# Optimization experiments

Measured on AMD Instinct MI355X. Metric: run time of the kernel, lower is better.

Reference implementation:

```python
import jax, jax.numpy as jnp
import numpy as np

B, C, H, W = 4, 64, 128, 128
NUM_HEAD = 1
SCALE = (C // NUM_HEAD) ** (-0.5)


def setup_inputs():
    key = jax.random.key(0)
    ks = jax.random.split(key, 32)
    def nrm(k, shape, s=0.05):
        return jax.random.normal(k, shape, jnp.float32) * s
    inp = {"x": jax.random.normal(ks[0], (B, C, H, W), jnp.float32)}
    i = 1
    for wn, bn in [("Wq", "bq"), ("Wk", "bk"), ("Wv", "bv"), ("Wl", "bl"), ("Wo", "bo"), ("Wp", "bp")]:
        inp[wn] = nrm(ks[i], (C, C)); i += 1
        inp[bn] = nrm(ks[i], (C,)); i += 1
    inp["sch_dw"] = nrm(ks[i], (C, 1, 5, 1)); i += 1
    inp["sch_dwb"] = nrm(ks[i], (C,)); i += 1
    inp["sch_pw"] = nrm(ks[i], (C, C, 1, 1)); i += 1
    inp["sch_pwb"] = nrm(ks[i], (C,)); i += 1
    inp["scv_dw"] = nrm(ks[i], (C, 1, 1, 5)); i += 1
    inp["scv_dwb"] = nrm(ks[i], (C,)); i += 1
    inp["scv_pw"] = nrm(ks[i], (C, C, 1, 1)); i += 1
    inp["scv_pwb"] = nrm(ks[i], (C,)); i += 1
    inp["convh_w"] = nrm(ks[i], (C, C, 1, 1)); i += 1
    inp["convh_b"] = nrm(ks[i], (C,)); i += 1
    inp["dsc_dw"] = nrm(ks[i], (C, 1, 3, 3)); i += 1
    inp["dsc_dwb"] = nrm(ks[i], (C,)); i += 1
    inp["dsc_pw"] = nrm(ks[i], (C, C, 1, 1)); i += 1
    inp["dsc_pwb"] = nrm(ks[i], (C,)); i += 1
    inp["ln_g"] = jnp.ones((C,), jnp.float32)
    inp["ln_b"] = jnp.zeros((C,), jnp.float32)
    return inp


def _linear(x, w, b):  # x [B,N,C], w [C,C] (torch Linear convention: y = x @ w.T + b)
    return x @ w.T + b


def _dwconv(x, w, b, pad):  # depthwise: x [B,C,H,W], w [C,1,kh,kw]
    y = jax.lax.conv_general_dilated(x, w, (1, 1), [(pad[0], pad[0]), (pad[1], pad[1])],
                                     dimension_numbers=("NCHW", "OIHW", "NCHW"),
                                     feature_group_count=x.shape[1])
    return y + b[None, :, None, None]


def _pwconv(x, w, b):  # 1x1 conv: w [Co,Ci,1,1]
    return jnp.einsum("bchw,oc->bohw", x, w[:, :, 0, 0]) + b[None, :, None, None]


def _attn(q, k, v):  # [B,N,C] each; dense NxN softmax attention
    a = jax.nn.softmax(jnp.einsum("bnc,bmc->bnm", q, k) * SCALE, axis=-1)
    return jnp.einsum("bnm,bmc->bnc", a, v)


def _up2_bilinear(x):  # bilinear, scale 2, align_corners=True
    Bb, Cc, Hh, Ww = x.shape
    def coords(n):
        s = jnp.linspace(0.0, n - 1.0, 2 * n)
        i0 = jnp.floor(s).astype(jnp.int32)
        i1 = jnp.minimum(i0 + 1, n - 1)
        return i0, i1, (s - i0).astype(x.dtype)
    y0, y1, wy = coords(Hh)
    x0, x1, wx = coords(Ww)
    r = x[:, :, y0, :] * (1.0 - wy)[None, None, :, None] + x[:, :, y1, :] * wy[None, None, :, None]
    return r[:, :, :, x0] * (1.0 - wx) + r[:, :, :, x1] * wx


def _forward(x, Wq, bq, Wk, bk, Wv, bv, Wl, bl, Wo, bo, Wp, bp,
             sch_dw, sch_dwb, sch_pw, sch_pwb, scv_dw, scv_dwb, scv_pw, scv_pwb,
             convh_w, convh_b, dsc_dw, dsc_dwb, dsc_pw, dsc_pwb, ln_g, ln_b):
    Bb, Cc, Hh, Ww = x.shape
    # AvgPool2d(2,2)
    xp = x.reshape(Bb, Cc, Hh // 2, 2, Ww // 2, 2).mean((3, 5))
    Hp, Wp_ = Hh // 2, Ww // 2
    N = Hp * Wp_
    # forward_lpg: GAP-gated self-attention producing low-freq prompt
    gap = xp.mean((2, 3), keepdims=True)
    xg = (gap * xp).reshape(Bb, Cc, N).transpose(0, 2, 1)  # [B,N,C]
    q = _linear(xg, Wq, bq); k = _linear(xg, Wk, bk); v = _linear(xg, Wv, bv)
    prompt_l = _linear(_attn(q, k, v), Wl, bl).transpose(0, 2, 1).reshape(Bb, Cc, Hp, Wp_)
    # forward_hpg: separable strip-conv branches -> high-freq prompt
    x_h = _pwconv(jax.nn.gelu(_dwconv(xp, sch_dw, sch_dwb, (2, 0)), approximate=False), sch_pw, sch_pwb)
    x_v = _pwconv(jax.nn.gelu(_dwconv(xp, scv_dw, scv_dwb, (0, 2)), approximate=False), scv_pw, scv_pwb)
    prompt_h = _pwconv(x_h + x_v, convh_w, convh_b)
    # forward_pgc: cross-attention Q=high, K=low, V=linear(x)
    x_V = _linear(xp.reshape(Bb, Cc, N).transpose(0, 2, 1), Wo, bo)
    x_K = prompt_l.reshape(Bb, Cc, N).transpose(0, 2, 1)
    x_Q = prompt_h.reshape(Bb, Cc, N).transpose(0, 2, 1)
    prompt = _attn(x_Q, x_K, x_V)
    prompt = _linear(prompt, Wp, bp) + x_V
    # LayerNorm over channel dim
    mu = prompt.mean(-1, keepdims=True)
    var = jnp.mean((prompt - mu) ** 2, axis=-1, keepdims=True)
    p_norm = (prompt - mu) / jnp.sqrt(var + 1e-5) * ln_g + ln_b
    p_norm = p_norm.transpose(0, 2, 1).reshape(Bb, Cc, Hp, Wp_)
    # dsc: depthwise 3x3 -> GELU -> 1x1, residual
    out = _pwconv(jax.nn.gelu(_dwconv(p_norm, dsc_dw, dsc_dwb, (1, 1)), approximate=False), dsc_pw, dsc_pwb) + p_norm
    return _up2_bilinear(out)


def reference(x, Wq, bq, Wk, bk, Wv, bv, Wl, bl, Wo, bo, Wp, bp,
              sch_dw, sch_dwb, sch_pw, sch_pwb, scv_dw, scv_dwb, scv_pw, scv_pwb,
              convh_w, convh_b, dsc_dw, dsc_dwb, dsc_pw, dsc_pwb, ln_g, ln_b):
    return _forward(x, Wq, bq, Wk, bk, Wv, bv, Wl, bl, Wo, bo, Wp, bp,
                    sch_dw, sch_dwb, sch_pw, sch_pwb, scv_dw, scv_dwb, scv_pw, scv_pwb,
                    convh_w, convh_b, dsc_dw, dsc_dwb, dsc_pw, dsc_pwb, ln_g, ln_b)
```

## Files before the change

### kernel.cpp

```cpp
#include <hip/hip_runtime.h>
#include <math.h>

#define Bn 4
#define Cn 64
#define Np 4096
#define NSPLIT 4
#define SCALE2 0.18033688011112042f

typedef unsigned short ushort_t;
typedef __attribute__((ext_vector_type(4))) float f32x4;
typedef __attribute__((ext_vector_type(8))) short bf16x8;
typedef __attribute__((ext_vector_type(4))) short bf16x4;

__device__ __forceinline__ float gelu_exact(float x) {
    return 0.5f * x * (1.0f + erff(x * 0.70710678118654752440f));
}
__device__ __forceinline__ ushort_t f2bf(float f) {
    unsigned int u = __float_as_uint(f);
    u += 0x7fffu + ((u >> 16) & 1u);
    return (ushort_t)(u >> 16);
}
__device__ __forceinline__ ushort_t f2bf_tr(float f) {
    return (ushort_t)(__float_as_uint(f) >> 16);
}
__device__ __forceinline__ float bf2f(ushort_t h) {
    return __uint_as_float(((unsigned int)h) << 16);
}
__device__ __forceinline__ void gload_lds16(const ushort_t* g, ushort_t* l) {
    __builtin_amdgcn_global_load_lds(
        (const __attribute__((address_space(1))) void*)g,
        (__attribute__((address_space(3))) void*)l, 16, 0, 0);
}
__device__ __forceinline__ bf16x8 cvt8(const float v[8]) {
    bf16x8 r;
    #pragma unroll
    for (int j = 0; j < 8; ++j) r[j] = (short)f2bf(v[j]);
    return r;
}
__device__ __forceinline__ void gemm16(const bf16x8 af[2], const float* __restrict__ W,
                                       int l16, int quad, f32x4* acc) {
    #pragma unroll
    for (int cb = 0; cb < 4; ++cb) {
        #pragma unroll
        for (int ks = 0; ks < 2; ++ks) {
            const float* p = W + (cb * 16 + l16) * 64 + ks * 32 + quad * 8;
            float v[8];
            #pragma unroll
            for (int j = 0; j < 8; ++j) v[j] = p[j];
            acc[cb] = __builtin_amdgcn_mfma_f32_16x16x32_bf16(af[ks], cvt8(v), acc[cb], 0, 0, 0);
        }
    }
}
__device__ __forceinline__ void gemm16T(const bf16x8 af[2], const float* __restrict__ W,
                                        int l16, int quad, f32x4* acc) {
    #pragma unroll
    for (int cb = 0; cb < 4; ++cb) {
        #pragma unroll
        for (int ks = 0; ks < 2; ++ks) {
            const float* p = W + (cb * 16 + l16) * 64 + ks * 32 + quad * 8;
            float v[8];
            #pragma unroll
            for (int j = 0; j < 8; ++j) v[j] = p[j];
            acc[cb] = __builtin_amdgcn_mfma_f32_16x16x32_bf16(cvt8(v), af[ks], acc[cb], 0, 0, 0);
        }
    }
}
__device__ __forceinline__ void aload(const float* xs, int row, int quad, bf16x8 af[2]) {
    #pragma unroll
    for (int ks = 0; ks < 2; ++ks) {
        float v[8];
        #pragma unroll
        for (int j = 0; j < 8; ++j) v[j] = xs[(ks * 32 + quad * 8 + j) * 65 + row];
        af[ks] = cvt8(v);
    }
}
__device__ __forceinline__ void stage_bchw(const float* __restrict__ X, int b, int n0, int t,
                                           float* xs) {
    #pragma unroll
    for (int u = 0; u < 16; ++u) {
        int idx = t + u * 256;
        int c = idx >> 6, nl = idx & 63;
        xs[c * 65 + nl] = X[((size_t)(b * Cn + c)) * Np + n0 + nl];
    }
}
__device__ __forceinline__ void stage_comb(const ushort_t* __restrict__ OpB, const float* linv,
                                           int b, int n0, int t, float* xs) {
    const size_t SS = (size_t)Bn * Np * Cn;
    int c4 = (t & 15) * 4;
    #pragma unroll
    for (int u = 0; u < 4; ++u) {
        int nl = (t >> 4) + u * 16;
        size_t gi = ((size_t)(b * Np + n0 + nl)) * Cn + c4;
        ushort4 a0 = *(const ushort4*)(OpB + gi);
        ushort4 a1 = *(const ushort4*)(OpB + SS + gi);
        ushort4 a2 = *(const ushort4*)(OpB + 2 * SS + gi);
        ushort4 a3 = *(const ushort4*)(OpB + 3 * SS + gi);
        float li = linv[nl];
        xs[(c4 + 0) * 65 + nl] = (bf2f(a0.x) + bf2f(a1.x) + bf2f(a2.x) + bf2f(a3.x)) * li;
        xs[(c4 + 1) * 65 + nl] = (bf2f(a0.y) + bf2f(a1.y) + bf2f(a2.y) + bf2f(a3.y)) * li;
        xs[(c4 + 2) * 65 + nl] = (bf2f(a0.z) + bf2f(a1.z) + bf2f(a2.z) + bf2f(a3.z)) * li;
        xs[(c4 + 3) * 65 + nl] = (bf2f(a0.w) + bf2f(a1.w) + bf2f(a2.w) + bf2f(a3.w)) * li;
    }
}
__device__ __forceinline__ void store_bnc_T(ushort_t* __restrict__ Y, int b, int n, int quad,
                                            const f32x4* acc, const float* __restrict__ bias,
                                            float mult) {
    #pragma unroll
    for (int cb = 0; cb < 4; ++cb) {
        int o0 = cb * 16 + quad * 4;
        ushort4 pk;
        pk.x = f2bf((acc[cb][0] + bias[o0 + 0]) * mult);
        pk.y = f2bf((acc[cb][1] + bias[o0 + 1]) * mult);
        pk.z = f2bf((acc[cb][2] + bias[o0 + 2]) * mult);
        pk.w = f2bf((acc[cb][3] + bias[o0 + 3]) * mult);
        *(ushort4*)(Y + ((size_t)(b * Np + n)) * Cn + o0) = pk;
    }
}
__device__ __forceinline__ void store_bchw_bf16(ushort_t* __restrict__ Y, int b, int nb, int l16,
                                                const f32x4* acc, const float* __restrict__ bias) {
    #pragma unroll
    for (int cb = 0; cb < 4; ++cb) {
        int col = cb * 16 + l16;
        float bb = bias[col];
        ushort4 pk;
        pk.x = f2bf(acc[cb][0] + bb); pk.y = f2bf(acc[cb][1] + bb);
        pk.z = f2bf(acc[cb][2] + bb); pk.w = f2bf(acc[cb][3] + bb);
        *(ushort4*)(Y + ((size_t)(b * Cn + col)) * Np + nb) = pk;
    }
}

__global__ void avgpool_kernel(const float* __restrict__ x, float* __restrict__ xp,
                               float* __restrict__ gap4k,
                               const float* __restrict__ convh_w, const float* __restrict__ convh_b,
                               const float* __restrict__ sch_pw, const float* __restrict__ sch_pwb,
                               const float* __restrict__ scv_pw, const float* __restrict__ scv_pwb,
                               float* __restrict__ Wc1, float* __restrict__ Wc2,
                               float* __restrict__ bcv) {
    if (blockIdx.x < 4096) {
        int idx = blockIdx.x * 256 + threadIdx.x;
        int j  = idx & 63;
        int i  = (idx >> 6) & 63;
        int bc = idx >> 12;
        const float* p = x + ((size_t)bc * 128 + 2 * i) * 128 + 2 * j;
        float v = 0.25f * (p[0] + p[1] + p[128] + p[129]);
        xp[idx] = v;
        float s = v;
        #pragma unroll
        for (int off = 1; off < 64; off <<= 1) s += __shfl_xor(s, off, 64);
        __shared__ float sm[4];
        if ((threadIdx.x & 63) == 0) sm[threadIdx.x >> 6] = s;
        __syncthreads();
        if (threadIdx.x == 0) gap4k[blockIdx.x] = sm[0] + sm[1] + sm[2] + sm[3];
    } else {
        int g = (blockIdx.x - 4096) * 256 + threadIdx.x;
        int sel = g >> 12, idx = g & 4095;
        int o = idx >> 6, c = idx & 63;
        const float* pw = sel ? scv_pw : sch_pw;
        float acc = 0.f;
        #pragma unroll 8
        for (int m = 0; m < 64; ++m) acc += convh_w[o * 64 + m] * pw[m * 64 + c];
        (sel ? Wc2 : Wc1)[idx] = acc * SCALE2;
        if (g < 64) {
            float ab = convh_b[g];
            for (int m = 0; m < 64; ++m) ab += convh_w[g * 64 + m] * (sch_pwb[m] + scv_pwb[m]);
            bcv[g] = ab * SCALE2;
        }
    }
}

__global__ __launch_bounds__(256) void qkv_dw_kernel(
    const float* __restrict__ xp, const float* __restrict__ gap4k,
    const float* __restrict__ Wq, const float* __restrict__ bq,
    const float* __restrict__ Wk, const float* __restrict__ bk,
    const float* __restrict__ Wv, const float* __restrict__ bv,
    const float* __restrict__ Wo, const float* __restrict__ bo,
    ushort_t* __restrict__ qb, ushort_t* __restrict__ kb, ushort_t* __restrict__ vb,
    float* __restrict__ xV, ushort_t* __restrict__ xVtb,
    const float* __restrict__ wv5, const float* __restrict__ bv5,
    const float* __restrict__ wh5, const float* __restrict__ bh5,
    ushort_t* __restrict__ gh, ushort_t* __restrict__ gv) {
    int b = blockIdx.y, t = threadIdx.x;
    if (blockIdx.x >= 64) {
        int part = blockIdx.x - 64;
        int e = part * 1024 + t * 4;
        size_t base = (size_t)b * (Cn * Np) + e;
        int c = e >> 12, i = (e >> 6) & 63, j = e & 63;
        const float* p = xp + ((size_t)(b * Cn + c)) * Np;
        float accV[4], accH[4];
        #pragma unroll
        for (int k = 0; k < 4; ++k) { accV[k] = bv5[c]; accH[k] = bh5[c]; }
        #pragma unroll
        for (int d = 0; d < 5; ++d) {
            int ii = i + d - 2;
            if (ii >= 0 && ii < 64) {
                f32x4 r = *(const f32x4*)(p + ii * 64 + j);
                float w = wv5[c * 5 + d];
                accV[0] += w * r[0]; accV[1] += w * r[1];
                accV[2] += w * r[2]; accV[3] += w * r[3];
            }
        }
        f32x4 c0 = *(const f32x4*)(p + i * 64 + j);
        float col[8];
        col[2] = c0[0]; col[3] = c0[1]; col[4] = c0[2]; col[5] = c0[3];
        col[0] = (j >= 2)     ? p[i * 64 + j - 2] : 0.f;
        col[1] = (j >= 1)     ? p[i * 64 + j - 1] : 0.f;
        col[6] = (j + 4 < 64) ? p[i * 64 + j + 4] : 0.f;
        col[7] = (j + 5 < 64) ? p[i * 64 + j + 5] : 0.f;
        #pragma unroll
        for (int k = 0; k < 4; ++k) {
            #pragma unroll
            for (int d = 0; d < 5; ++d) accH[k] += wh5[c * 5 + d] * col[k + d];
        }
        ushort4 ph, pv_;
        ph.x = f2bf(gelu_exact(accV[0])); ph.y = f2bf(gelu_exact(accV[1]));
        ph.z = f2bf(gelu_exact(accV[2])); ph.w = f2bf(gelu_exact(accV[3]));
        pv_.x = f2bf(gelu_exact(accH[0])); pv_.y = f2bf(gelu_exact(accH[1]));
        pv_.z = f2bf(gelu_exact(accH[2])); pv_.w = f2bf(gelu_exact(accH[3]));
        *(ushort4*)(gh + base) = ph;
        *(ushort4*)(gv + base) = pv_;
        return;
    }
    __shared__ float xs[64 * 65];
    __shared__ float gl[64];
    int n0 = blockIdx.x * 64;
    int wv_ = t >> 6, lane = t & 63, l16 = lane & 15, quad = lane >> 4;
    stage_bchw(xp, b, n0, t, xs);
    if (t < 64) {
        float s = 0.f;
        #pragma unroll
        for (int u = 0; u < 16; ++u) s += gap4k[(b * 64 + t) * 16 + u];
        gl[t] = s * (1.f / 4096.f);
    }
    __syncthreads();
    int row = wv_ * 16 + l16;
    int n   = n0 + wv_ * 16 + l16;
    int nb  = n0 + wv_ * 16 + quad * 4;
    bf16x8 ar[2], ag[2];
    #pragma unroll
    for (int ks = 0; ks < 2; ++ks) {
        float vr[8], vg[8];
        #pragma unroll
        for (int j = 0; j < 8; ++j) {
            int k = ks * 32 + quad * 8 + j;
            float xv = xs[k * 65 + row];
            vr[j] = xv; vg[j] = xv * gl[k];
        }
        ar[ks] = cvt8(vr); ag[ks] = cvt8(vg);
    }
    f32x4 acc[4];
    #pragma unroll
    for (int cb = 0; cb < 4; ++cb) acc[cb] = (f32x4){0.f, 0.f, 0.f, 0.f};
    gemm16T(ag, Wq, l16, quad, acc);
    store_bnc_T(qb, b, n, quad, acc, bq, SCALE2);
    #pragma unroll
    for (int cb = 0; cb < 4; ++cb) acc[cb] = (f32x4){0.f, 0.f, 0.f, 0.f};
    gemm16T(ag, Wk, l16, quad, acc);
    store_bnc_T(kb, b, n, quad, acc, bk, 1.f);
    #pragma unroll
    for (int cb = 0; cb < 4; ++cb) acc[cb] = (f32x4){0.f, 0.f, 0.f, 0.f};
    gemm16(ag, Wv, l16, quad, acc);
    store_bchw_bf16(vb, b, nb, l16, acc, bv);
    #pragma unroll
    for (int cb = 0; cb < 4; ++cb) acc[cb] = (f32x4){0.f, 0.f, 0.f, 0.f};
    gemm16(ar, Wo, l16, quad, acc);
    #pragma unroll
    for (int cb = 0; cb < 4; ++cb) {
        int col = cb * 16 + l16;
        float bb = bo[col];
        ushort4 pk;
        float y0 = acc[cb][0] + bb, y1 = acc[cb][1] + bb, y2 = acc[cb][2] + bb, y3 = acc[cb][3] + bb;
        xV[((size_t)(b * Np + nb + 0)) * Cn + col] = y0;
        xV[((size_t)(b * Np + nb + 1)) * Cn + col] = y1;
        xV[((size_t)(b * Np + nb + 2)) * Cn + col] = y2;
        xV[((size_t)(b * Np + nb + 3)) * Cn + col] = y3;
        pk.x = f2bf(y0); pk.y = f2bf(y1); pk.z = f2bf(y2); pk.w = f2bf(y3);
        *(ushort4*)(xVtb + ((size_t)(b * Cn + col)) * Np + nb) = pk;
    }
}

__device__ __forceinline__ void attn_body(
    int xblk, int b, const ushort_t* __restrict__ Qb, const ushort_t* __restrict__ Kb,
    const ushort_t* __restrict__ Vtb, ushort_t* __restrict__ OpB, float* __restrict__ Lpart,
    ushort_t* smem) {
    ushort_t* kt0 = smem;
    ushort_t* vt0 = smem + 8192;
    int split = xblk >> 6;
    int qt    = xblk & 63;
    int n0    = qt * 64;
    int t     = threadIdx.x;
    int wave  = t >> 6, lane = t & 63;
    int l16   = lane & 15, quad = lane >> 4;
    int lrow  = lane >> 3;
    int kvbase = split * (Np / NSPLIT);

    const ushort_t* qp = Qb + ((size_t)(b * Np) + n0 + wave * 16 + l16) * Cn + quad * 8;
    bf16x8 aq0 = *(const bf16x8*)(qp);
    bf16x8 aq1 = *(const bf16x8*)(qp + 32);

    f32x4 oa[4];
    float psum = 0.f;
    #pragma unroll
    for (int db = 0; db < 4; ++db) oa[db] = (f32x4){0.f, 0.f, 0.f, 0.f};

    int wh  = wave & 1;
    int jsw = ((lane & 7) ^ lrow) & 7;
    const ushort_t* gK  = Kb + ((size_t)b * Np + kvbase + wh * 32 + lrow) * Cn + jsw * 8;
    const ushort_t* gV0 = Vtb + ((size_t)(b * Cn) + wh * 32 + lrow) * Np + kvbase + jsw * 8;
    const ushort_t* gV1 = gV0 + (size_t)8 * Np;
    const ushort_t* gV2 = gV0 + (size_t)16 * Np;
    const ushort_t* gV3 = gV0 + (size_t)24 * Np;
    ushort_t* ldK = kt0 + wh * 2048;
    ushort_t* ldV = vt0 + wh * 2048;

    const ushort_t* kr0 = kt0 + l16 * 64 + ((quad ^ (l16 & 7)) & 7) * 8;
    const ushort_t* kr1 = kt0 + l16 * 64 + (((quad + 4) ^ (l16 & 7)) & 7) * 8;
    int h = quad >> 1, q1 = quad & 1, e = l16 & 7;
    const ushort_t* vr0 = vt0 + l16 * 64 + (((0 + h) ^ e) & 7) * 8 + q1 * 4;
    const ushort_t* vr1 = vt0 + l16 * 64 + (((2 + h) ^ e) & 7) * 8 + q1 * 4;
    const ushort_t* vr2 = vt0 + l16 * 64 + (((4 + h) ^ e) & 7) * 8 + q1 * 4;
    const ushort_t* vr3 = vt0 + l16 * 64 + (((6 + h) ^ e) & 7) * 8 + q1 * 4;

    auto stage = [&](int buf) {
        if (wave < 2) {
            ushort_t* dst = ldK + buf * 4096;
            gload_lds16(gK,        dst);
            gload_lds16(gK + 512,  dst + 512);
            gload_lds16(gK + 1024, dst + 1024);
            gload_lds16(gK + 1536, dst + 1536);
            gK += 64 * Cn;
        } else {
            ushort_t* dst = ldV + buf * 4096;
            gload_lds16(gV0, dst);
            gload_lds16(gV1, dst + 512);
            gload_lds16(gV2, dst + 1024);
            gload_lds16(gV3, dst + 1536);
            gV0 += 64; gV1 += 64; gV2 += 64; gV3 += 64;
        }
    };

    auto compute = [&](int B2) {
        const int ko = B2 * 4096;
        f32x4 sa[4];
        #pragma unroll
        for (int cb = 0; cb < 4; ++cb) sa[cb] = (f32x4){0.f, 0.f, 0.f, 0.f};
        #pragma unroll
        for (int cb = 0; cb < 4; ++cb) {
            bf16x8 bk0 = *(const bf16x8*)(kr0 + ko + cb * 1024);
            bf16x8 bk1 = *(const bf16x8*)(kr1 + ko + cb * 1024);
            sa[cb] = __builtin_amdgcn_mfma_f32_16x16x32_bf16(bk0, aq0, sa[cb], 0, 0, 0);
            sa[cb] = __builtin_amdgcn_mfma_f32_16x16x32_bf16(bk1, aq1, sa[cb], 0, 0, 0);
        }
        bf16x4 pb[4];
        #pragma unroll
        for (int cb = 0; cb < 4; ++cb) {
            float p0 = exp2f(sa[cb][0]), p1 = exp2f(sa[cb][1]);
            float p2 = exp2f(sa[cb][2]), p3 = exp2f(sa[cb][3]);
            psum += (p0 + p1) + (p2 + p3);
            bf16x4 pk;
            pk[0] = (short)f2bf_tr(p0); pk[1] = (short)f2bf_tr(p1);
            pk[2] = (short)f2bf_tr(p2); pk[3] = (short)f2bf_tr(p3);
            pb[cb] = pk;
        }
        #pragma unroll
        for (int db = 0; db < 4; ++db) {
            bf16x4 a0 = *(const bf16x4*)(vr0 + ko + db * 1024);
            bf16x4 a1 = *(const bf16x4*)(vr1 + ko + db * 1024);
            bf16x4 a2 = *(const bf16x4*)(vr2 + ko + db * 1024);
            bf16x4 a3 = *(const bf16x4*)(vr3 + ko + db * 1024);
            oa[db] = __builtin_amdgcn_mfma_f32_16x16x16bf16_1k(a0, pb[0], oa[db], 0, 0, 0);
            oa[db] = __builtin_amdgcn_mfma_f32_16x16x16bf16_1k(a1, pb[1], oa[db], 0, 0, 0);
            oa[db] = __builtin_amdgcn_mfma_f32_16x16x16bf16_1k(a2, pb[2], oa[db], 0, 0, 0);
            oa[db] = __builtin_amdgcn_mfma_f32_16x16x16bf16_1k(a3, pb[3], oa[db], 0, 0, 0);
        }
        __syncthreads();
    };

    const int NT = (Np / NSPLIT) / 64;
    stage(0);
    __syncthreads();
    #pragma unroll 1
    for (int mm = 0; mm < NT / 2; ++mm) {
        stage(1);
        compute(0);
        if (mm < NT / 2 - 1) stage(0);
        compute(1);
    }

    psum += __shfl_xor(psum, 16, 64);
    psum += __shfl_xor(psum, 32, 64);
    size_t obase = ((size_t)(split * Bn + b)) * Np;
    int n = n0 + wave * 16 + l16;
    if (quad == 0) Lpart[obase + n] = psum;
    #pragma unroll
    for (int db = 0; db < 4; ++db) {
        ushort4 pk;
        pk.x = f2bf(oa[db][0]); pk.y = f2bf(oa[db][1]);
        pk.z = f2bf(oa[db][2]); pk.w = f2bf(oa[db][3]);
        *(ushort4*)(OpB + (obase + n) * Cn + db * 16 + quad * 4) = pk;
    }
}

__device__ __forceinline__ void hpg_body(
    int tile, int b, const ushort_t* __restrict__ gh, const ushort_t* __restrict__ gv,
    const float* __restrict__ Wc1, const float* __restrict__ Wc2, const float* __restrict__ bcv,
    ushort_t* __restrict__ xQb, ushort_t* smem) {
    ushort_t* xs1 = smem;
    ushort_t* xs2 = smem + 4608;
    int n0 = tile * 64, t = threadIdx.x;
    int wv_ = t >> 6, lane = t & 63, l16 = lane & 15, quad = lane >> 4;
    #pragma unroll
    for (int u = 0; u < 4; ++u) {
        int lin = u * 256 + t;
        int c = lin >> 4, nl4 = (lin & 15) * 4;
        size_t gi = ((size_t)(b * Cn + c)) * Np + n0 + nl4;
        ushort4 g1 = *(const ushort4*)(gh + gi);
        ushort4 g2 = *(const ushort4*)(gv + gi);
        xs1[(nl4 + 0) * 72 + c] = g1.x; xs1[(nl4 + 1) * 72 + c] = g1.y;
        xs1[(nl4 + 2) * 72 + c] = g1.z; xs1[(nl4 + 3) * 72 + c] = g1.w;
        xs2[(nl4 + 0) * 72 + c] = g2.x; xs2[(nl4 + 1) * 72 + c] = g2.y;
        xs2[(nl4 + 2) * 72 + c] = g2.z; xs2[(nl4 + 3) * 72 + c] = g2.w;
    }
    __syncthreads();
    int row = wv_ * 16 + l16;
    bf16x8 a1[2], a2[2];
    #pragma unroll
    for (int ks = 0; ks < 2; ++ks) {
        a1[ks] = *(const bf16x8*)(xs1 + row * 72 + ks * 32 + quad * 8);
        a2[ks] = *(const bf16x8*)(xs2 + row * 72 + ks * 32 + quad * 8);
    }
    f32x4 acc[4];
    #pragma unroll
    for (int cb = 0; cb < 4; ++cb) acc[cb] = (f32x4){0.f, 0.f, 0.f, 0.f};
    gemm16T(a1, Wc1, l16, quad, acc);
    gemm16T(a2, Wc2, l16, quad, acc);
    store_bnc_T(xQb, b, n0 + wv_ * 16 + l16, quad, acc, bcv, 1.f);
}

__global__ __launch_bounds__(256) void attn_hpg_kernel(
    const ushort_t* __restrict__ Qb, const ushort_t* __restrict__ Kb,
    const ushort_t* __restrict__ Vtb, ushort_t* __restrict__ OpB, float* __restrict__ Lpart,
    const ushort_t* __restrict__ gh, const ushort_t* __restrict__ gv,
    const float* __restrict__ Wc1, const float* __restrict__ Wc2,
    const float* __restrict__ bcv, ushort_t* __restrict__ xQb) {
    __shared__ ushort_t smem[16384];
    int b = blockIdx.y;
    if (blockIdx.x < 256)
        attn_body(blockIdx.x, b, Qb, Kb, Vtb, OpB, Lpart, smem);
    else
        hpg_body(blockIdx.x - 256, b, gh, gv, Wc1, Wc2, bcv, xQb, smem);
}

__global__ __launch_bounds__(256) void wl_mfma(
    const ushort_t* __restrict__ OpB, const float* __restrict__ Lp,
    const float* __restrict__ Wl, const float* __restrict__ bl, ushort_t* __restrict__ xKb) {
    __shared__ float xs[64 * 65];
    __shared__ float linv[64];
    int b = blockIdx.y, n0 = blockIdx.x * 64, t = threadIdx.x;
    int wv_ = t >> 6, lane = t & 63, l16 = lane & 15, quad = lane >> 4;
    if (t < 64) {
        size_t li = (size_t)b * Np + n0 + t;
        const size_t LS = (size_t)Bn * Np;
        linv[t] = 1.f / (Lp[li] + Lp[LS + li] + Lp[2 * LS + li] + Lp[3 * LS + li]);
    }
    __syncthreads();
    stage_comb(OpB, linv, b, n0, t, xs);
    __syncthreads();
    bf16x8 af[2];
    aload(xs, wv_ * 16 + l16, quad, af);
    f32x4 acc[4];
    #pragma unroll
    for (int cb = 0; cb < 4; ++cb) acc[cb] = (f32x4){0.f, 0.f, 0.f, 0.f};
    gemm16T(af, Wl, l16, quad, acc);
    store_bnc_T(xKb, b, n0 + wv_ * 16 + l16, quad, acc, bl, 1.f);
}

__global__ __launch_bounds__(256) void linln_mfma(
    const ushort_t* __restrict__ OpB, const float* __restrict__ Lp,
    const float* __restrict__ Wp, const float* __restrict__ bp,
    const float* __restrict__ xV, const float* __restrict__ g, const float* __restrict__ beta,
    float* __restrict__ out) {
    __shared__ float xs[64 * 65];
    __shared__ float linv[64];
    int b = blockIdx.y, n0 = blockIdx.x * 64, t = threadIdx.x;
    int wv_ = t >> 6, lane = t & 63, l16 = lane & 15, quad = lane >> 4;
    if (t < 64) {
        size_t li = (size_t)b * Np + n0 + t;
        const size_t LS = (size_t)Bn * Np;
        linv[t] = 1.f / (Lp[li] + Lp[LS + li] + Lp[2 * LS + li] + Lp[3 * LS + li]);
    }
    __syncthreads();
    stage_comb(OpB, linv, b, n0, t, xs);
    __syncthreads();
    bf16x8 af[2];
    aload(xs, wv_ * 16 + l16, quad, af);
    f32x4 acc[4];
    #pragma unroll
    for (int cb = 0; cb < 4; ++cb) acc[cb] = (f32x4){0.f, 0.f, 0.f, 0.f};
    gemm16(af, Wp, l16, quad, acc);
    int nb = n0 + wv_ * 16 + quad * 4;
    float vals[4][4], gc[4], bec[4];
    #pragma unroll
    for (int cb = 0; cb < 4; ++cb) {
        int col = cb * 16 + l16;
        float bb = bp[col];
        gc[cb] = g[col]; bec[cb] = beta[col];
        #pragma unroll
        for (int r = 0; r < 4; ++r)
            vals[cb][r] = acc[cb][r] + bb + xV[((size_t)(b * Np + nb + r)) * Cn + col];
    }
    f32x4 yn[4];
    #pragma unroll
    for (int r = 0; r < 4; ++r) {
        float s = 0.f, s2 = 0.f;
        #pragma unroll
        for (int cb = 0; cb < 4; ++cb) { s += vals[cb][r]; s2 += vals[cb][r] * vals[cb][r]; }
        #pragma unroll
        for (int off = 1; off < 16; off <<= 1) {
            s  += __shfl_xor(s, off, 64);
            s2 += __shfl_xor(s2, off, 64);
        }
        float mu  = s * (1.f / 64.f);
        float var = s2 * (1.f / 64.f) - mu * mu;
        float ivs = rsqrtf(var + 1e-5f);
        #pragma unroll
        for (int cb = 0; cb < 4; ++cb)
            yn[cb][r] = (vals[cb][r] - mu) * ivs * gc[cb] + bec[cb];
    }
    #pragma unroll
    for (int cb = 0; cb < 4; ++cb)
        *(f32x4*)(out + ((size_t)(b * Cn + cb * 16 + l16)) * Np + nb) = yn[cb];
}

__global__ __launch_bounds__(256) void dsc_mfma(
    const float* __restrict__ X, const float* __restrict__ dw, const float* __restrict__ dwb,
    const float* __restrict__ W, const float* __restrict__ bias, float* __restrict__ out) {
    __shared__ float xs[64 * 65];
    int b = blockIdx.y, irow = blockIdx.x, n0 = irow * 64, t = threadIdx.x;
    int wv_ = t >> 6, lane = t & 63, l16 = lane & 15, quad = lane >> 4;
    int j = t & 63;
    #pragma unroll
    for (int u = 0; u < 16; ++u) {
        int c = (t >> 6) + u * 4;
        const float* p = X + ((size_t)(b * Cn + c)) * Np + n0;
        float acc = dwb[c];
        #pragma unroll
        for (int dy = 0; dy < 3; ++dy) {
            int ii = irow + dy - 1;
            if (ii < 0 || ii >= 64) continue;
            const float* pr = p + (dy - 1) * 64;
            #pragma unroll
            for (int dx = 0; dx < 3; ++dx) {
                int jj = j + dx - 1;
                if (jj < 0 || jj >= 64) continue;
                acc += dw[c * 9 + dy * 3 + dx] * pr[jj];
            }
        }
        xs[c * 65 + j] = gelu_exact(acc);
    }
    __syncthreads();
    bf16x8 af[2];
    aload(xs, wv_ * 16 + l16, quad, af);
    f32x4 acc[4];
    #pragma unroll
    for (int cb = 0; cb < 4; ++cb) acc[cb] = (f32x4){0.f, 0.f, 0.f, 0.f};
    gemm16(af, W, l16, quad, acc);
    int nb = n0 + wv_ * 16 + quad * 4;
    #pragma unroll
    for (int cb = 0; cb < 4; ++cb) {
        int col = cb * 16 + l16;
        float bb = bias[col];
        size_t oi = ((size_t)(b * Cn + col)) * Np + nb;
        f32x4 rv = *(const f32x4*)(X + oi);
        f32x4 v4;
        #pragma unroll
        for (int r = 0; r < 4; ++r) v4[r] = acc[cb][r] + bb + rv[r];
        *(f32x4*)(out + oi) = v4;
    }
}

__global__ void upsample_kernel(const float* __restrict__ in, float* __restrict__ out) {
    int idx = blockIdx.x * 256 + threadIdx.x;
    int x4 = (idx & 31) * 4;
    int y  = (idx >> 5) & 127;
    int bc = idx >> 12;
    float sy = y * (63.f / 127.f);
    int y0 = (int)sy;
    float fy = sy - y0;
    int y1 = min(y0 + 1, 63);
    const float* p0 = in + (size_t)bc * Np + y0 * 64;
    const float* p1 = in + (size_t)bc * Np + y1 * 64;
    f32x4 o;
    #pragma unroll
    for (int k = 0; k < 4; ++k) {
        int xo = x4 + k;
        float sx = xo * (63.f / 127.f);
        int x0 = (int)sx;
        float fx = sx - x0;
        int x1 = min(x0 + 1, 63);
        float r0 = p0[x0] + (p0[x1] - p0[x0]) * fx;
        float r1 = p1[x0] + (p1[x1] - p1[x0]) * fx;
        o[k] = r0 + (r1 - r0) * fy;
    }
    *(f32x4*)(out + (size_t)idx * 4) = o;
}

extern "C" void kernel_launch(void* const* d_in, const int* in_sizes, int n_in,
                              void* d_out, int out_size, void* d_ws, size_t ws_size,
                              hipStream_t stream) {
    const float* x       = (const float*)d_in[0];
    const float* Wq      = (const float*)d_in[1];
    const float* bq      = (const float*)d_in[2];
    const float* Wk      = (const float*)d_in[3];
    const float* bk      = (const float*)d_in[4];
    const float* Wv      = (const float*)d_in[5];
    const float* bv      = (const float*)d_in[6];
    const float* Wl      = (const float*)d_in[7];
    const float* bl      = (const float*)d_in[8];
    const float* Wo      = (const float*)d_in[9];
    const float* bo      = (const float*)d_in[10];
    const float* Wp      = (const float*)d_in[11];
    const float* bp      = (const float*)d_in[12];
    const float* sch_dw  = (const float*)d_in[13];
    const float* sch_dwb = (const float*)d_in[14];
    const float* sch_pw  = (const float*)d_in[15];
    const float* sch_pwb = (const float*)d_in[16];
    const float* scv_dw  = (const float*)d_in[17];
    const float* scv_dwb = (const float*)d_in[18];
    const float* scv_pw  = (const float*)d_in[19];
    const float* scv_pwb = (const float*)d_in[20];
    const float* convh_w = (const float*)d_in[21];
    const float* convh_b = (const float*)d_in[22];
    const float* dsc_dw  = (const float*)d_in[23];
    const float* dsc_dwb = (const float*)d_in[24];
    const float* dsc_pw  = (const float*)d_in[25];
    const float* dsc_pwb = (const float*)d_in[26];
    const float* ln_g    = (const float*)d_in[27];
    const float* ln_b    = (const float*)d_in[28];

    float* ws = (float*)d_ws;
    const size_t SZ = (size_t)Bn * Np * Cn;
    float* xp   = ws;
    float* xV   = ws + SZ;
    ushort_t* ghb = (ushort_t*)(ws + 2 * SZ);
    ushort_t* gh  = ghb;
    ushort_t* gv  = ghb + SZ;
    float* f2   = ws + 2 * SZ;
    ushort_t* bws  = (ushort_t*)(ws + 3 * SZ);
    ushort_t* qb   = bws;
    ushort_t* kb_  = bws + SZ;
    ushort_t* vb   = bws + 2 * SZ;
    ushort_t* xKb  = bws + 3 * SZ;
    ushort_t* xVtb = bws + 4 * SZ;
    ushort_t* xQb  = bws + 5 * SZ;
    ushort_t* OpB  = (ushort_t*)(ws + 6 * SZ);
    float* gap4k  = ws + 8 * SZ;
    float* Lpart  = gap4k + 4096;
    float* Wc1  = Lpart + (size_t)NSPLIT * Bn * Np;
    float* Wc2  = Wc1 + 4096;
    float* bcv  = Wc2 + 4096;

    dim3 g64(64, Bn);

    avgpool_kernel<<<4096 + 32, 256, 0, stream>>>(x, xp, gap4k,
                                                  convh_w, convh_b, sch_pw, sch_pwb,
                                                  scv_pw, scv_pwb, Wc1, Wc2, bcv);
    qkv_dw_kernel<<<dim3(64 + 256, Bn), 256, 0, stream>>>(
        xp, gap4k, Wq, bq, Wk, bk, Wv, bv, Wo, bo,
        qb, kb_, vb, xV, xVtb, sch_dw, sch_dwb, scv_dw, scv_dwb, gh, gv);
    attn_hpg_kernel<<<dim3(256 + 64, Bn), 256, 0, stream>>>(
        qb, kb_, vb, OpB, Lpart, gh, gv, Wc1, Wc2, bcv, xQb);
    wl_mfma<<<g64, 256, 0, stream>>>(OpB, Lpart, Wl, bl, xKb);
    attn_hpg_kernel<<<dim3(256, Bn), 256, 0, stream>>>(
        xQb, xKb, xVtb, OpB, Lpart, gh, gv, Wc1, Wc2, bcv, xQb);
    linln_mfma<<<g64, 256, 0, stream>>>(OpB, Lpart, Wp, bp, xV, ln_g, ln_b, xp);
    dsc_mfma<<<g64, 256, 0, stream>>>(xp, dsc_dw, dsc_dwb, dsc_pw, dsc_pwb, f2);
    upsample_kernel<<<4096, 256, 0, stream>>>(f2, (float*)d_out);
}
```

Before: 265.1 us.

## Double attention query tile per block and pre-convert weights to bf16

The attention body now processes 128 query rows per block, so each wave handles two 16-row query tiles that share every K/V fragment loaded from shared memory. This halves the number of attention blocks and the K/V staging traffic per query. Separately, all 64x64 projection weights are converted to bf16 once in the first kernel, so GEMMs load packed bf16 vectors instead of eight floats followed by a conversion. The cost is higher register pressure from the doubled accumulators, which may lower occupancy, and fewer blocks to fill the device.

```diff
diff --git a/kernel.cpp b/kernel.cpp
--- a/kernel.cpp
+++ b/kernel.cpp
@@ -37,31 +37,25 @@
     for (int j = 0; j < 8; ++j) r[j] = (short)f2bf(v[j]);
     return r;
 }
-__device__ __forceinline__ void gemm16(const bf16x8 af[2], const float* __restrict__ W,
-                                       int l16, int quad, f32x4* acc) {
+__device__ __forceinline__ void gemm16b(const bf16x8 af[2], const ushort_t* __restrict__ Wb,
+                                        int l16, int quad, f32x4* acc) {
     #pragma unroll
     for (int cb = 0; cb < 4; ++cb) {
         #pragma unroll
         for (int ks = 0; ks < 2; ++ks) {
-            const float* p = W + (cb * 16 + l16) * 64 + ks * 32 + quad * 8;
-            float v[8];
-            #pragma unroll
-            for (int j = 0; j < 8; ++j) v[j] = p[j];
-            acc[cb] = __builtin_amdgcn_mfma_f32_16x16x32_bf16(af[ks], cvt8(v), acc[cb], 0, 0, 0);
-        }
-    }
-}
-__device__ __forceinline__ void gemm16T(const bf16x8 af[2], const float* __restrict__ W,
-                                        int l16, int quad, f32x4* acc) {
+            bf16x8 bw = *(const bf16x8*)(Wb + (cb * 16 + l16) * 64 + ks * 32 + quad * 8);
+            acc[cb] = __builtin_amdgcn_mfma_f32_16x16x32_bf16(af[ks], bw, acc[cb], 0, 0, 0);
+        }
+    }
+}
+__device__ __forceinline__ void gemm16Tb(const bf16x8 af[2], const ushort_t* __restrict__ Wb,
+                                         int l16, int quad, f32x4* acc) {
     #pragma unroll
     for (int cb = 0; cb < 4; ++cb) {
         #pragma unroll
         for (int ks = 0; ks < 2; ++ks) {
-            const float* p = W + (cb * 16 + l16) * 64 + ks * 32 + quad * 8;
-            float v[8];
-            #pragma unroll
-            for (int j = 0; j < 8; ++j) v[j] = p[j];
-            acc[cb] = __builtin_amdgcn_mfma_f32_16x16x32_bf16(cvt8(v), af[ks], acc[cb], 0, 0, 0);
+            bf16x8 bw = *(const bf16x8*)(Wb + (cb * 16 + l16) * 64 + ks * 32 + quad * 8);
+            acc[cb] = __builtin_amdgcn_mfma_f32_16x16x32_bf16(bw, af[ks], acc[cb], 0, 0, 0);
         }
     }
 }
@@ -134,8 +128,12 @@
                                const float* __restrict__ convh_w, const float* __restrict__ convh_b,
                                const float* __restrict__ sch_pw, const float* __restrict__ sch_pwb,
                                const float* __restrict__ scv_pw, const float* __restrict__ scv_pwb,
-                               float* __restrict__ Wc1, float* __restrict__ Wc2,
-                               float* __restrict__ bcv) {
+                               ushort_t* __restrict__ Wc1b, ushort_t* __restrict__ Wc2b,
+                               float* __restrict__ bcv,
+                               const float* __restrict__ Wq, const float* __restrict__ Wk,
+                               const float* __restrict__ Wv, const float* __restrict__ Wo,
+                               const float* __restrict__ Wl, const float* __restrict__ Wp,
+                               const float* __restrict__ dscpw, ushort_t* __restrict__ Wball) {
     if (blockIdx.x < 4096) {
         int idx = blockIdx.x * 256 + threadIdx.x;
         int j  = idx & 63;
@@ -151,7 +149,7 @@
         if ((threadIdx.x & 63) == 0) sm[threadIdx.x >> 6] = s;
         __syncthreads();
         if (threadIdx.x == 0) gap4k[blockIdx.x] = sm[0] + sm[1] + sm[2] + sm[3];
-    } else {
+    } else if (blockIdx.x < 4128) {
         int g = (blockIdx.x - 4096) * 256 + threadIdx.x;
         int sel = g >> 12, idx = g & 4095;
         int o = idx >> 6, c = idx & 63;
@@ -159,21 +157,26 @@
         float acc = 0.f;
         #pragma unroll 8
         for (int m = 0; m < 64; ++m) acc += convh_w[o * 64 + m] * pw[m * 64 + c];
-        (sel ? Wc2 : Wc1)[idx] = acc * SCALE2;
+        (sel ? Wc2b : Wc1b)[idx] = f2bf(acc * SCALE2);
         if (g < 64) {
             float ab = convh_b[g];
             for (int m = 0; m < 64; ++m) ab += convh_w[g * 64 + m] * (sch_pwb[m] + scv_pwb[m]);
             bcv[g] = ab * SCALE2;
         }
+    } else {
+        int g = (blockIdx.x - 4128) * 256 + threadIdx.x;
+        int which = g >> 12, idx = g & 4095;
+        const float* srcs[7] = {Wq, Wk, Wv, Wo, Wl, Wp, dscpw};
+        Wball[g] = f2bf(srcs[which][idx]);
     }
 }
 
 __global__ __launch_bounds__(256) void qkv_dw_kernel(
     const float* __restrict__ xp, const float* __restrict__ gap4k,
-    const float* __restrict__ Wq, const float* __restrict__ bq,
-    const float* __restrict__ Wk, const float* __restrict__ bk,
-    const float* __restrict__ Wv, const float* __restrict__ bv,
-    const float* __restrict__ Wo, const float* __restrict__ bo,
+    const ushort_t* __restrict__ Wqb, const float* __restrict__ bq,
+    const ushort_t* __restrict__ Wkb, const float* __restrict__ bk,
+    const ushort_t* __restrict__ Wvb, const float* __restrict__ bv,
+    const ushort_t* __restrict__ Wob, const float* __restrict__ bo,
     ushort_t* __restrict__ qb, ushort_t* __restrict__ kb, ushort_t* __restrict__ vb,
     float* __restrict__ xV, ushort_t* __restrict__ xVtb,
     const float* __restrict__ wv5, const float* __restrict__ bv5,
@@ -250,19 +253,19 @@
     f32x4 acc[4];
     #pragma unroll
     for (int cb = 0; cb < 4; ++cb) acc[cb] = (f32x4){0.f, 0.f, 0.f, 0.f};
-    gemm16T(ag, Wq, l16, quad, acc);
+    gemm16Tb(ag, Wqb, l16, quad, acc);
     store_bnc_T(qb, b, n, quad, acc, bq, SCALE2);
     #pragma unroll
     for (int cb = 0; cb < 4; ++cb) acc[cb] = (f32x4){0.f, 0.f, 0.f, 0.f};
-    gemm16T(ag, Wk, l16, quad, acc);
+    gemm16Tb(ag, Wkb, l16, quad, acc);
     store_bnc_T(kb, b, n, quad, acc, bk, 1.f);
     #pragma unroll
     for (int cb = 0; cb < 4; ++cb) acc[cb] = (f32x4){0.f, 0.f, 0.f, 0.f};
-    gemm16(ag, Wv, l16, quad, acc);
+    gemm16b(ag, Wvb, l16, quad, acc);
     store_bchw_bf16(vb, b, nb, l16, acc, bv);
     #pragma unroll
     for (int cb = 0; cb < 4; ++cb) acc[cb] = (f32x4){0.f, 0.f, 0.f, 0.f};
-    gemm16(ar, Wo, l16, quad, acc);
+    gemm16b(ar, Wob, l16, quad, acc);
     #pragma unroll
     for (int cb = 0; cb < 4; ++cb) {
         int col = cb * 16 + l16;
@@ -284,23 +287,28 @@
     ushort_t* smem) {
     ushort_t* kt0 = smem;
     ushort_t* vt0 = smem + 8192;
-    int split = xblk >> 6;
-    int qt    = xblk & 63;
-    int n0    = qt * 64;
+    int split = xblk >> 5;
+    int qt    = xblk & 31;
+    int n0    = qt * 128;
     int t     = threadIdx.x;
     int wave  = t >> 6, lane = t & 63;
     int l16   = lane & 15, quad = lane >> 4;
     int lrow  = lane >> 3;
     int kvbase = split * (Np / NSPLIT);
 
-    const ushort_t* qp = Qb + ((size_t)(b * Np) + n0 + wave * 16 + l16) * Cn + quad * 8;
-    bf16x8 aq0 = *(const bf16x8*)(qp);
-    bf16x8 aq1 = *(const bf16x8*)(qp + 32);
-
-    f32x4 oa[4];
-    float psum = 0.f;
-    #pragma unroll
-    for (int db = 0; db < 4; ++db) oa[db] = (f32x4){0.f, 0.f, 0.f, 0.f};
+    const ushort_t* qp = Qb + ((size_t)(b * Np) + n0 + wave * 32 + l16) * Cn + quad * 8;
+    bf16x8 aq00 = *(const bf16x8*)(qp);
+    bf16x8 aq01 = *(const bf16x8*)(qp + 32);
+    bf16x8 aq10 = *(const bf16x8*)(qp + 16 * Cn);
+    bf16x8 aq11 = *(const bf16x8*)(qp + 16 * Cn + 32);
+
+    f32x4 oa0[4], oa1[4];
+    float psum0 = 0.f, psum1 = 0.f;
+    #pragma unroll
+    for (int db = 0; db < 4; ++db) {
+        oa0[db] = (f32x4){0.f, 0.f, 0.f, 0.f};
+        oa1[db] = (f32x4){0.f, 0.f, 0.f, 0.f};
+    }
 
     int wh  = wave & 1;
     int jsw = ((lane & 7) ^ lrow) & 7;
@@ -340,26 +348,38 @@
 
     auto compute = [&](int B2) {
         const int ko = B2 * 4096;
-        f32x4 sa[4];
-        #pragma unroll
-        for (int cb = 0; cb < 4; ++cb) sa[cb] = (f32x4){0.f, 0.f, 0.f, 0.f};
+        f32x4 sa0[4], sa1[4];
+        #pragma unroll
+        for (int cb = 0; cb < 4; ++cb) {
+            sa0[cb] = (f32x4){0.f, 0.f, 0.f, 0.f};
+            sa1[cb] = (f32x4){0.f, 0.f, 0.f, 0.f};
+        }
         #pragma unroll
         for (int cb = 0; cb < 4; ++cb) {
             bf16x8 bk0 = *(const bf16x8*)(kr0 + ko + cb * 1024);
             bf16x8 bk1 = *(const bf16x8*)(kr1 + ko + cb * 1024);
-            sa[cb] = __builtin_amdgcn_mfma_f32_16x16x32_bf16(bk0, aq0, sa[cb], 0, 0, 0);
-            sa[cb] = __builtin_amdgcn_mfma_f32_16x16x32_bf16(bk1, aq1, sa[cb], 0, 0, 0);
-        }
-        bf16x4 pb[4];
+            sa0[cb] = __builtin_amdgcn_mfma_f32_16x16x32_bf16(bk0, aq00, sa0[cb], 0, 0, 0);
+            sa0[cb] = __builtin_amdgcn_mfma_f32_16x16x32_bf16(bk1, aq01, sa0[cb], 0, 0, 0);
+            sa1[cb] = __builtin_amdgcn_mfma_f32_16x16x32_bf16(bk0, aq10, sa1[cb], 0, 0, 0);
+            sa1[cb] = __builtin_amdgcn_mfma_f32_16x16x32_bf16(bk1, aq11, sa1[cb], 0, 0, 0);
+        }
+        bf16x4 pb0[4], pb1[4];
         #pragma unroll
         for (int cb = 0; cb < 4; ++cb) {
-            float p0 = exp2f(sa[cb][0]), p1 = exp2f(sa[cb][1]);
-            float p2 = exp2f(sa[cb][2]), p3 = exp2f(sa[cb][3]);
-            psum += (p0 + p1) + (p2 + p3);
+            float p0 = exp2f(sa0[cb][0]), p1 = exp2f(sa0[cb][1]);
+            float p2 = exp2f(sa0[cb][2]), p3 = exp2f(sa0[cb][3]);
+            psum0 += (p0 + p1) + (p2 + p3);
             bf16x4 pk;
             pk[0] = (short)f2bf_tr(p0); pk[1] = (short)f2bf_tr(p1);
             pk[2] = (short)f2bf_tr(p2); pk[3] = (short)f2bf_tr(p3);
-            pb[cb] = pk;
+            pb0[cb] = pk;
+            float q0 = exp2f(sa1[cb][0]), q1f = exp2f(sa1[cb][1]);
+            float q2 = exp2f(sa1[cb][2]), q3 = exp2f(sa1[cb][3]);
+            psum1 += (q0 + q1f) + (q2 + q3);
+            bf16x4 qk;
+            qk[0] = (short)f2bf_tr(q0); qk[1] = (short)f2bf_tr(q1f);
+            qk[2] = (short)f2bf_tr(q2); qk[3] = (short)f2bf_tr(q3);
+            pb1[cb] = qk;
         }
         #pragma unroll
         for (int db = 0; db < 4; ++db) {
@@ -367,10 +387,14 @@
             bf16x4 a1 = *(const bf16x4*)(vr1 + ko + db * 1024);
             bf16x4 a2 = *(const bf16x4*)(vr2 + ko + db * 1024);
             bf16x4 a3 = *(const bf16x4*)(vr3 + ko + db * 1024);
-            oa[db] = __builtin_amdgcn_mfma_f32_16x16x16bf16_1k(a0, pb[0], oa[db], 0, 0, 0);
-            oa[db] = __builtin_amdgcn_mfma_f32_16x16x16bf16_1k(a1, pb[1], oa[db], 0, 0, 0);
-            oa[db] = __builtin_amdgcn_mfma_f32_16x16x16bf16_1k(a2, pb[2], oa[db], 0, 0, 0);
-            oa[db] = __builtin_amdgcn_mfma_f32_16x16x16bf16_1k(a3, pb[3], oa[db], 0, 0, 0);
+            oa0[db] = __builtin_amdgcn_mfma_f32_16x16x16bf16_1k(a0, pb0[0], oa0[db], 0, 0, 0);
+            oa0[db] = __builtin_amdgcn_mfma_f32_16x16x16bf16_1k(a1, pb0[1], oa0[db], 0, 0, 0);
+            oa0[db] = __builtin_amdgcn_mfma_f32_16x16x16bf16_1k(a2, pb0[2], oa0[db], 0, 0, 0);
+            oa0[db] = __builtin_amdgcn_mfma_f32_16x16x16bf16_1k(a3, pb0[3], oa0[db], 0, 0, 0);
+            oa1[db] = __builtin_amdgcn_mfma_f32_16x16x16bf16_1k(a0, pb1[0], oa1[db], 0, 0, 0);
+            oa1[db] = __builtin_amdgcn_mfma_f32_16x16x16bf16_1k(a1, pb1[1], oa1[db], 0, 0, 0);
+            oa1[db] = __builtin_amdgcn_mfma_f32_16x16x16bf16_1k(a2, pb1[2], oa1[db], 0, 0, 0);
+            oa1[db] = __builtin_amdgcn_mfma_f32_16x16x16bf16_1k(a3, pb1[3], oa1[db], 0, 0, 0);
         }
         __syncthreads();
     };
@@ -386,23 +410,33 @@
         compute(1);
     }
 
-    psum += __shfl_xor(psum, 16, 64);
-    psum += __shfl_xor(psum, 32, 64);
+    psum0 += __shfl_xor(psum0, 16, 64);
+    psum0 += __shfl_xor(psum0, 32, 64);
+    psum1 += __shfl_xor(psum1, 16, 64);
+    psum1 += __shfl_xor(psum1, 32, 64);
     size_t obase = ((size_t)(split * Bn + b)) * Np;
-    int n = n0 + wave * 16 + l16;
-    if (quad == 0) Lpart[obase + n] = psum;
+    int n = n0 + wave * 32 + l16;
+    if (quad == 0) {
+        Lpart[obase + n]      = psum0;
+        Lpart[obase + n + 16] = psum1;
+    }
     #pragma unroll
     for (int db = 0; db < 4; ++db) {
         ushort4 pk;
-        pk.x = f2bf(oa[db][0]); pk.y = f2bf(oa[db][1]);
-        pk.z = f2bf(oa[db][2]); pk.w = f2bf(oa[db][3]);
+        pk.x = f2bf(oa0[db][0]); pk.y = f2bf(oa0[db][1]);
+        pk.z = f2bf(oa0[db][2]); pk.w = f2bf(oa0[db][3]);
         *(ushort4*)(OpB + (obase + n) * Cn + db * 16 + quad * 4) = pk;
+        ushort4 qk;
+        qk.x = f2bf(oa1[db][0]); qk.y = f2bf(oa1[db][1]);
+        qk.z = f2bf(oa1[db][2]); qk.w = f2bf(oa1[db][3]);
+        *(ushort4*)(OpB + (obase + n + 16) * Cn + db * 16 + quad * 4) = qk;
     }
 }
 
 __device__ __forceinline__ void hpg_body(
     int tile, int b, const ushort_t* __restrict__ gh, const ushort_t* __restrict__ gv,
-    const float* __restrict__ Wc1, const float* __restrict__ Wc2, const float* __restrict__ bcv,
+    const ushort_t* __restrict__ Wc1b, const ushort_t* __restrict__ Wc2b,
+    const float* __restrict__ bcv,
     ushort_t* __restrict__ xQb, ushort_t* smem) {
     ushort_t* xs1 = smem;
     ushort_t* xs2 = smem + 4608;
@@ -431,8 +465,8 @@
     f32x4 acc[4];
     #pragma unroll
     for (int cb = 0; cb < 4; ++cb) acc[cb] = (f32x4){0.f, 0.f, 0.f, 0.f};
-    gemm16T(a1, Wc1, l16, quad, acc);
-    gemm16T(a2, Wc2, l16, quad, acc);
+    gemm16Tb(a1, Wc1b, l16, quad, acc);
+    gemm16Tb(a2, Wc2b, l16, quad, acc);
     store_bnc_T(xQb, b, n0 + wv_ * 16 + l16, quad, acc, bcv, 1.f);
 }
 
@@ -440,19 +474,19 @@
     const ushort_t* __restrict__ Qb, const ushort_t* __restrict__ Kb,
     const ushort_t* __restrict__ Vtb, ushort_t* __restrict__ OpB, float* __restrict__ Lpart,
     const ushort_t* __restrict__ gh, const ushort_t* __restrict__ gv,
-    const float* __restrict__ Wc1, const float* __restrict__ Wc2,
+    const ushort_t* __restrict__ Wc1b, const ushort_t* __restrict__ Wc2b,
     const float* __restrict__ bcv, ushort_t* __restrict__ xQb) {
     __shared__ ushort_t smem[16384];
     int b = blockIdx.y;
-    if (blockIdx.x < 256)
+    if (blockIdx.x < 128)
         attn_body(blockIdx.x, b, Qb, Kb, Vtb, OpB, Lpart, smem);
     else
-        hpg_body(blockIdx.x - 256, b, gh, gv, Wc1, Wc2, bcv, xQb, smem);
+        hpg_body(blockIdx.x - 128, b, gh, gv, Wc1b, Wc2b, bcv, xQb, smem);
 }
 
 __global__ __launch_bounds__(256) void wl_mfma(
     const ushort_t* __restrict__ OpB, const float* __restrict__ Lp,
-    const float* __restrict__ Wl, const float* __restrict__ bl, ushort_t* __restrict__ xKb) {
+    const ushort_t* __restrict__ Wlb, const float* __restrict__ bl, ushort_t* __restrict__ xKb) {
     __shared__ float xs[64 * 65];
     __shared__ float linv[64];
     int b = blockIdx.y, n0 = blockIdx.x * 64, t = threadIdx.x;
@@ -470,13 +504,13 @@
     f32x4 acc[4];
     #pragma unroll
     for (int cb = 0; cb < 4; ++cb) acc[cb] = (f32x4){0.f, 0.f, 0.f, 0.f};
-    gemm16T(af, Wl, l16, quad, acc);
+    gemm16Tb(af, Wlb, l16, quad, acc);
     store_bnc_T(xKb, b, n0 + wv_ * 16 + l16, quad, acc, bl, 1.f);
 }
 
 __global__ __launch_bounds__(256) void linln_mfma(
     const ushort_t* __restrict__ OpB, const float* __restrict__ Lp,
-    const float* __restrict__ Wp, const float* __restrict__ bp,
+    const ushort_t* __restrict__ Wpb, const float* __restrict__ bp,
     const float* __restrict__ xV, const float* __restrict__ g, const float* __restrict__ beta,
     float* __restrict__ out) {
     __shared__ float xs[64 * 65];
@@ -496,7 +530,7 @@
     f32x4 acc[4];
     #pragma unroll
     for (int cb = 0; cb < 4; ++cb) acc[cb] = (f32x4){0.f, 0.f, 0.f, 0.f};
-    gemm16(af, Wp, l16, quad, acc);
+    gemm16b(af, Wpb, l16, quad, acc);
     int nb = n0 + wv_ * 16 + quad * 4;
     float vals[4][4], gc[4], bec[4];
     #pragma unroll
@@ -533,7 +567,7 @@
 
 __global__ __launch_bounds__(256) void dsc_mfma(
     const float* __restrict__ X, const float* __restrict__ dw, const float* __restrict__ dwb,
-    const float* __restrict__ W, const float* __restrict__ bias, float* __restrict__ out) {
+    const ushort_t* __restrict__ Wb, const float* __restrict__ bias, float* __restrict__ out) {
     __shared__ float xs[64 * 65];
     int b = blockIdx.y, irow = blockIdx.x, n0 = irow * 64, t = threadIdx.x;
     int wv_ = t >> 6, lane = t & 63, l16 = lane & 15, quad = lane >> 4;
@@ -563,7 +597,7 @@
     f32x4 acc[4];
     #pragma unroll
     for (int cb = 0; cb < 4; ++cb) acc[cb] = (f32x4){0.f, 0.f, 0.f, 0.f};
-    gemm16(af, W, l16, quad, acc);
+    gemm16b(af, Wb, l16, quad, acc);
     int nb = n0 + wv_ * 16 + quad * 4;
     #pragma unroll
     for (int cb = 0; cb < 4; ++cb) {
@@ -655,24 +689,34 @@
     ushort_t* OpB  = (ushort_t*)(ws + 6 * SZ);
     float* gap4k  = ws + 8 * SZ;
     float* Lpart  = gap4k + 4096;
-    float* Wc1  = Lpart + (size_t)NSPLIT * Bn * Np;
-    float* Wc2  = Wc1 + 4096;
-    float* bcv  = Wc2 + 4096;
+    float* wcslot = Lpart + (size_t)NSPLIT * Bn * Np;
+    ushort_t* Wc1b = (ushort_t*)wcslot;
+    ushort_t* Wc2b = Wc1b + 4096;
+    float* bcv  = wcslot + 4096;
+    ushort_t* Wball = (ushort_t*)(bcv + 64);
+    ushort_t* Wqb   = Wball;
+    ushort_t* Wkb   = Wball + 4096;
+    ushort_t* Wvb   = Wball + 8192;
+    ushort_t* Wob   = Wball + 12288;
+    ushort_t* Wlb   = Wball + 16384;
+    ushort_t* Wpb   = Wball + 20480;
+    ushort_t* Wdscb = Wball + 24576;
 
     dim3 g64(64, Bn);
 
-    avgpool_kernel<<<4096 + 32, 256, 0, stream>>>(x, xp, gap4k,
+    avgpool_kernel<<<4096 + 32 + 112, 256, 0, stream>>>(x, xp, gap4k,
                                                   convh_w, convh_b, sch_pw, sch_pwb,
-                                                  scv_pw, scv_pwb, Wc1, Wc2, bcv);
+                                                  scv_pw, scv_pwb, Wc1b, Wc2b, bcv,
+                                                  Wq, Wk, Wv, Wo, Wl, Wp, dsc_pw, Wball);
     qkv_dw_kernel<<<dim3(64 + 256, Bn), 256, 0, stream>>>(
-        xp, gap4k, Wq, bq, Wk, bk, Wv, bv, Wo, bo,
+        xp, gap4k, Wqb, bq, Wkb, bk, Wvb, bv, Wob, bo,
         qb, kb_, vb, xV, xVtb, sch_dw, sch_dwb, scv_dw, scv_dwb, gh, gv);
-    attn_hpg_kernel<<<dim3(256 + 64, Bn), 256, 0, stream>>>(
-        qb, kb_, vb, OpB, Lpart, gh, gv, Wc1, Wc2, bcv, xQb);
-    wl_mfma<<<g64, 256, 0, stream>>>(OpB, Lpart, Wl, bl, xKb);
-    attn_hpg_kernel<<<dim3(256, Bn), 256, 0, stream>>>(
-        xQb, xKb, xVtb, OpB, Lpart, gh, gv, Wc1, Wc2, bcv, xQb);
-    linln_mfma<<<g64, 256, 0, stream>>>(OpB, Lpart, Wp, bp, xV, ln_g, ln_b, xp);
-    dsc_mfma<<<g64, 256, 0, stream>>>(xp, dsc_dw, dsc_dwb, dsc_pw, dsc_pwb, f2);
+    attn_hpg_kernel<<<dim3(128 + 64, Bn), 256, 0, stream>>>(
+        qb, kb_, vb, OpB, Lpart, gh, gv, Wc1b, Wc2b, bcv, xQb);
+    wl_mfma<<<g64, 256, 0, stream>>>(OpB, Lpart, Wlb, bl, xKb);
+    attn_hpg_kernel<<<dim3(128, Bn), 256, 0, stream>>>(
+        xQb, xKb, xVtb, OpB, Lpart, gh, gv, Wc1b, Wc2b, bcv, xQb);
+    linln_mfma<<<g64, 256, 0, stream>>>(OpB, Lpart, Wpb, bp, xV, ln_g, ln_b, xp);
+    dsc_mfma<<<g64, 256, 0, stream>>>(xp, dsc_dw, dsc_dwb, Wdscb, dsc_pwb, f2);
     upsample_kernel<<<4096, 256, 0, stream>>>(f2, (float*)d_out);
 }
```

Result: no change. 264.0 us (-0.4%).
